# Optimization experiments

Measured on AMD Instinct MI355X. Metric: run time of the kernel, lower is better.

Reference implementation:

```python
import jax, jax.numpy as jnp
import numpy as np

B, S, F = 8, 1024, 512
E, H = 64, 16  # embed_dim per head, n_heads (match init_kwargs)


def setup_inputs() -> dict:
    key = jax.random.key(0)
    k1, k2, k3, k4, k5, k6 = jax.random.split(key, 6)
    inputs1 = jax.random.normal(k1, (B, S, F), dtype=jnp.float32)
    inputs2 = jax.random.normal(k2, (B, S, F), dtype=jnp.float32)
    W_kv = jax.random.normal(k3, (F, E * H * 2), dtype=jnp.float32) * 0.02
    b_kv = jax.random.normal(k4, (E * H * 2,), dtype=jnp.float32) * 0.02
    W_q = jax.random.normal(k5, (F, E * H), dtype=jnp.float32) * 0.02
    b_q = jax.random.normal(k6, (E * H,), dtype=jnp.float32) * 0.02
    return {"inputs1": inputs1, "inputs2": inputs2,
            "W_kv": W_kv, "b_kv": b_kv, "W_q": W_q, "b_q": b_q}


def reference(inputs1, inputs2, W_kv, b_kv, W_q, b_q):
    scaling = 1.0 / jnp.sqrt(jnp.float32(E))
    # KV path: Dense then reshape (B,S,E,H,2) -> transpose to (B,2,H,S,E)
    kv = inputs1 @ W_kv + b_kv                      # (B,S,E*H*2), layout d-major
    kv = kv.reshape(B, S, E, H, 2)
    kv = jnp.transpose(kv, (0, 4, 3, 1, 2))        # (B,2,H,S,E)
    k = kv[:, 0]                                   # (B,H,S,E)
    v = kv[:, 1]                                   # (B,H,S,E)
    # Q path: Dense then reshape (B,S,E,H) -> (B,H,S,E)
    q = (inputs2 @ W_q + b_q).reshape(B, S, E, H)
    q = jnp.transpose(q, (0, 3, 1, 2))             # (B,H,S,E)
    # Attention: softmax FIRST, then scale (non-standard, faithful to source)
    qk = jnp.einsum('bhqe,bhke->bhqk', q, k)       # (B,H,S,S)
    attn = jax.nn.softmax(qk, axis=-1) * scaling
    out = jnp.einsum('bhqk,bhke->bhqe', attn, v)   # (B,H,S,E)
    out = jnp.transpose(out, (0, 2, 1, 3))         # (B,S,H,E)
    return out.reshape(B, S, E * H)
```

## Files before the change

### kernel.cpp

```cpp
#include <hip/hip_runtime.h>
#include <hip/hip_bf16.h>
#include <math.h>

#define NB 8
#define NS 1024
#define NF 512
#define NE 64
#define NH 16

typedef __attribute__((ext_vector_type(8))) short short8;
typedef __attribute__((ext_vector_type(4))) float floatx4;

__device__ inline unsigned short f2bf(float f) {
  union { float f; unsigned int u; } c; c.f = f;
  unsigned int u = c.u;
  u += 0x7FFFu + ((u >> 16) & 1u);
  return (unsigned short)(u >> 16);
}

__device__ inline unsigned int cvt_pk_bf16(float a, float b) {
  unsigned int r;
  asm("v_cvt_pk_bf16_f32 %0, %1, %2" : "=v"(r) : "v"(a), "v"(b));
  return r;
}

__device__ inline float fexp2(float x) {
#if __has_builtin(__builtin_amdgcn_exp2f)
  return __builtin_amdgcn_exp2f(x);
#else
  return exp2f(x);
#endif
}

__device__ inline void gl_lds16(const void* g, void* l) {
  __builtin_amdgcn_global_load_lds(
      (const __attribute__((address_space(1))) unsigned int*)g,
      (__attribute__((address_space(3))) unsigned int*)l, 16, 0, 0);
}

__global__ __launch_bounds__(256) void conv_bf16(
    const float* __restrict__ in, unsigned short* __restrict__ out, int n4)
{
  int i = blockIdx.x * 256 + threadIdx.x;
  if (i < n4) {
    float4 v = ((const float4*)in)[i];
    ushort4 o;
    o.x = f2bf(v.x); o.y = f2bf(v.y); o.z = f2bf(v.z); o.w = f2bf(v.w);
    ((ushort4*)out)[i] = o;
  }
}

template <int LOGG>
__global__ __launch_bounds__(256) void perm_w(
    const float* __restrict__ W, unsigned short* __restrict__ Wt, int N)
{
  __shared__ float T[64][65];
  const int t = threadIdx.x;
  const int k0 = blockIdx.y * 64, n0 = blockIdx.x * 64;
  #pragma unroll
  for (int p = 0; p < 4; ++p) {
    int i = (t >> 4) + p * 16, j = (t & 15) * 4;
    float4 v = *(const float4*)(W + (size_t)(k0 + i) * N + n0 + j);
    T[i][j] = v.x; T[i][j + 1] = v.y; T[i][j + 2] = v.z; T[i][j + 3] = v.w;
  }
  __syncthreads();
  #pragma unroll
  for (int p = 0; p < 2; ++p) {
    int c = p * 256 + t;
    int jn = c >> 3, kc = (c & 7) * 8;
    int n = n0 + jn;
    int g = n & ((1 << LOGG) - 1), e = n >> LOGG;
    unsigned short v[8];
    #pragma unroll
    for (int j = 0; j < 8; ++j) v[j] = f2bf(T[kc + j][jn]);
    *(uint4*)(Wt + (size_t)(g * 64 + e) * NF + k0 + kc) = *(uint4*)v;
  }
}

template <int MODE>
__global__ __launch_bounds__(256) void gemm_proj(
    const unsigned short* __restrict__ A, const unsigned short* __restrict__ Wt,
    const float* __restrict__ bias, unsigned short* __restrict__ out0,
    unsigned short* __restrict__ out1)
{
  __shared__ union {
    struct { unsigned short A[2][128 * 32]; unsigned short B[2][128 * 32]; } ab;
    unsigned short C[128 * 136];
    struct { unsigned short K[128][72]; unsigned short V[64][136]; } kv;
  } u;

  const int t = threadIdx.x;
  const int w = t >> 6, l = t & 63;
  const int quad = l >> 4, l16 = l & 15;
  const int n0 = blockIdx.x * 128, m0 = blockIdx.y * 128;
  const int wm = (w >> 1) * 64, wn = (w & 1) * 64;

  floatx4 acc[4][4];
  #pragma unroll
  for (int mi = 0; mi < 4; ++mi)
    #pragma unroll
    for (int nj = 0; nj < 4; ++nj) acc[mi][nj] = (floatx4){0.f, 0.f, 0.f, 0.f};

  const unsigned short* Ag = A + (size_t)(m0 + w * 16 + (l >> 2)) * NF + (l & 3) * 8;
  const unsigned short* Bg = Wt + (size_t)(n0 + w * 16 + (l >> 2)) * NF + (l & 3) * 8;

  gl_lds16(Ag,           &u.ab.A[0][(w * 16) * 32]);
  gl_lds16(Ag + 64 * NF, &u.ab.A[0][(64 + w * 16) * 32]);
  gl_lds16(Bg,           &u.ab.B[0][(w * 16) * 32]);
  gl_lds16(Bg + 64 * NF, &u.ab.B[0][(64 + w * 16) * 32]);

  for (int kt = 0; kt < 16; ++kt) {
    __syncthreads();
    const int cur = kt & 1;
    if (kt < 15) {
      const int k0 = (kt + 1) * 32;
      gl_lds16(Ag + k0,           &u.ab.A[cur ^ 1][(w * 16) * 32]);
      gl_lds16(Ag + 64 * NF + k0, &u.ab.A[cur ^ 1][(64 + w * 16) * 32]);
      gl_lds16(Bg + k0,           &u.ab.B[cur ^ 1][(w * 16) * 32]);
      gl_lds16(Bg + 64 * NF + k0, &u.ab.B[cur ^ 1][(64 + w * 16) * 32]);
    }
    short8 af[4], bf[4];
    #pragma unroll
    for (int mi = 0; mi < 4; ++mi)
      af[mi] = *(const short8*)&u.ab.A[cur][(wm + mi * 16 + l16) * 32 + quad * 8];
    #pragma unroll
    for (int nj = 0; nj < 4; ++nj)
      bf[nj] = *(const short8*)&u.ab.B[cur][(wn + nj * 16 + l16) * 32 + quad * 8];
    #pragma unroll
    for (int mi = 0; mi < 4; ++mi)
      #pragma unroll
      for (int nj = 0; nj < 4; ++nj)
        acc[mi][nj] = __builtin_amdgcn_mfma_f32_16x16x32_bf16(
            af[mi], bf[nj], acc[mi][nj], 0, 0, 0);
  }

  float bv[4];
  #pragma unroll
  for (int nj = 0; nj < 4; ++nj) {
    int np = n0 + wn + nj * 16 + l16;
    int n = (MODE == 0) ? ((np & 63) * 32 + (np >> 6)) : ((np & 63) * 16 + (np >> 6));
    bv[nj] = bias[n];
  }
  __syncthreads();

  if (MODE == 0) {
    if (wn == 0) {
      #pragma unroll
      for (int mi = 0; mi < 4; ++mi)
        #pragma unroll
        for (int nj = 0; nj < 4; ++nj)
          #pragma unroll
          for (int r = 0; r < 4; ++r)
            u.kv.K[wm + mi * 16 + quad * 4 + r][nj * 16 + l16] =
                f2bf(acc[mi][nj][r] + bv[nj]);
    } else {
      #pragma unroll
      for (int mi = 0; mi < 4; ++mi)
        #pragma unroll
        for (int nj = 0; nj < 4; ++nj)
          #pragma unroll
          for (int r = 0; r < 4; ++r)
            u.kv.V[nj * 16 + l16][wm + mi * 16 + quad * 4 + r] =
                f2bf(acc[mi][nj][r] + bv[nj]);
    }
  } else {
    const float LOG2E = 1.44269504088896f;
    #pragma unroll
    for (int mi = 0; mi < 4; ++mi)
      #pragma unroll
      for (int nj = 0; nj < 4; ++nj)
        #pragma unroll
        for (int r = 0; r < 4; ++r)
          u.C[(wm + mi * 16 + quad * 4 + r) * 136 + wn + nj * 16 + l16] =
              f2bf((acc[mi][nj][r] + bv[nj]) * LOG2E);
  }
  __syncthreads();

  if (MODE == 0) {
    const int h = n0 >> 7, btile = m0 >> 10, s0 = m0 & 1023;
    #pragma unroll
    for (int p = 0; p < 4; ++p) {
      int c = p * 256 + t;
      int m = c >> 3, ec = c & 7;
      uint4 v = *(const uint4*)&u.kv.K[m][ec * 8];
      *(uint4*)(out0 + (((size_t)btile * NH + h) * NS + s0 + m) * NE + ec * 8) = v;
    }
    #pragma unroll
    for (int p = 0; p < 4; ++p) {
      int c = p * 256 + t;
      int e = c >> 4, mc = c & 15;
      uint4 v = *(const uint4*)&u.kv.V[e][mc * 8];
      *(uint4*)(out1 + (((size_t)btile * NH + h) * NE + e) * NS + s0 + mc * 8) = v;
    }
  } else {
    #pragma unroll
    for (int p = 0; p < 8; ++p) {
      int c = p * 256 + t;
      int m = c >> 4, col8 = (c & 15) * 8;
      uint4 v = *(const uint4*)&u.C[m * 136 + col8];
      int mg = m0 + m, b = mg >> 10, s = mg & 1023;
      int h = (n0 >> 6) + (col8 >> 6), e0 = col8 & 63;
      *(uint4*)(out0 + (((size_t)b * NH + h) * NS + s) * NE + e0) = v;
    }
  }
}

__global__ __launch_bounds__(256) void attn_kernel(
    const unsigned short* __restrict__ Q, const unsigned short* __restrict__ K,
    const unsigned short* __restrict__ Vt, float* __restrict__ out)
{
  __shared__ unsigned short Ks[2][64][64];
  __shared__ unsigned short Vs[2][64][64];

  const int t = threadIdx.x;
  const int w = t >> 6, lane = t & 63;
  const int quad = lane >> 4, l16 = lane & 15;
  const int n = blockIdx.x;
  const int qt = n >> 7;
  const int g = n & 127;
  const int h = g & 15, b = g >> 4;
  const size_t bh = ((size_t)b * NH + h) * NS * NE;

  short8 aq[2][2];
  #pragma unroll
  for (int rb = 0; rb < 2; ++rb) {
    const unsigned short* qrow =
        Q + bh + (size_t)(qt * 128 + w * 32 + rb * 16 + l16) * NE;
    aq[rb][0] = *(const short8*)(qrow + quad * 8);
    aq[rb][1] = *(const short8*)(qrow + 32 + quad * 8);
  }

  const int sr = t >> 3, sc8 = t & 7;
  const int xs = (sc8 ^ (sr & 7)) * 8;
  const int xq = (quad ^ (l16 & 7)) * 8;
  const unsigned short* Kg = K + bh;
  const unsigned short* Vg = Vt + bh;

  {
    *(uint4*)&Ks[0][sr][xs]      = *(const uint4*)(Kg + (size_t)sr * NE + sc8 * 8);
    *(uint4*)&Ks[0][32 + sr][xs] = *(const uint4*)(Kg + (size_t)(32 + sr) * NE + sc8 * 8);
    *(uint4*)&Vs[0][sr][xs]      = *(const uint4*)(Vg + (size_t)sr * NS + sc8 * 8);
    *(uint4*)&Vs[0][32 + sr][xs] = *(const uint4*)(Vg + (size_t)(32 + sr) * NS + sc8 * 8);
  }

  float lsum[2] = {0.f, 0.f};
  floatx4 O[2][4];
  #pragma unroll
  for (int rb = 0; rb < 2; ++rb)
    #pragma unroll
    for (int j = 0; j < 4; ++j) O[rb][j] = (floatx4){0.f, 0.f, 0.f, 0.f};

  for (int kt = 0; kt < NS / 64; ++kt) {
    __syncthreads();
    const int bi = kt & 1;

    uint4 kn0, kn1, vn0, vn1;
    if (kt < 15) {
      const unsigned short* kg = Kg + (size_t)(kt + 1) * 64 * NE;
      kn0 = *(const uint4*)(kg + (size_t)sr * NE + sc8 * 8);
      kn1 = *(const uint4*)(kg + (size_t)(32 + sr) * NE + sc8 * 8);
      const unsigned short* vg = Vg + (kt + 1) * 64;
      vn0 = *(const uint4*)(vg + (size_t)sr * NS + sc8 * 8);
      vn1 = *(const uint4*)(vg + (size_t)(32 + sr) * NS + sc8 * 8);
    }

    short8 kf0[4], kf1[4];
    #pragma unroll
    for (int kb = 0; kb < 4; ++kb) {
      kf0[kb] = *(const short8*)&Ks[bi][kb * 16 + l16][xq];
      kf1[kb] = *(const short8*)&Ks[bi][kb * 16 + l16][xq ^ 32];
    }

    short8 paf[2][2];
    #pragma unroll
    for (int rb = 0; rb < 2; ++rb) {
      floatx4 st[4];
      __builtin_amdgcn_s_setprio(1);
      #pragma unroll
      for (int kb = 0; kb < 4; ++kb) {
        floatx4 z = (floatx4){0.f, 0.f, 0.f, 0.f};
        z = __builtin_amdgcn_mfma_f32_16x16x32_bf16(kf0[kb], aq[rb][0], z, 0, 0, 0);
        st[kb] = __builtin_amdgcn_mfma_f32_16x16x32_bf16(kf1[kb], aq[rb][1], z, 0, 0, 0);
      }
      __builtin_amdgcn_s_setprio(0);
      unsigned int c[4][2];
      #pragma unroll
      for (int kb = 0; kb < 4; ++kb) {
        float p0 = fexp2(st[kb][0]), p1 = fexp2(st[kb][1]);
        float p2 = fexp2(st[kb][2]), p3 = fexp2(st[kb][3]);
        lsum[rb] += (p0 + p1) + (p2 + p3);
        c[kb][0] = cvt_pk_bf16(p0, p1);
        c[kb][1] = cvt_pk_bf16(p2, p3);
      }
      #pragma unroll
      for (int m = 0; m < 2; ++m) {
        union { unsigned int wd[4]; short8 v; } pu;
        #pragma unroll
        for (int j = 0; j < 2; ++j) {
          unsigned int a = c[2 * m][j], bb = c[2 * m + 1][j];
          asm("v_permlane32_swap_b32 %0, %1" : "+v"(a), "+v"(bb));
          asm("v_permlane16_swap_b32 %0, %1" : "+v"(a), "+v"(bb));
          pu.wd[j]     = a;
          pu.wd[2 + j] = bb;
        }
        paf[rb][m] = pu.v;
      }
    }

    if (kt < 15) {
      const int bn = bi ^ 1;
      *(uint4*)&Ks[bn][sr][xs]      = kn0;
      *(uint4*)&Ks[bn][32 + sr][xs] = kn1;
      *(uint4*)&Vs[bn][sr][xs]      = vn0;
      *(uint4*)&Vs[bn][32 + sr][xs] = vn1;
    }

    short8 vf0[4], vf1[4];
    #pragma unroll
    for (int eb = 0; eb < 4; ++eb) {
      vf0[eb] = *(const short8*)&Vs[bi][eb * 16 + l16][xq];
      vf1[eb] = *(const short8*)&Vs[bi][eb * 16 + l16][xq ^ 32];
    }
    __builtin_amdgcn_s_setprio(1);
    #pragma unroll
    for (int rb = 0; rb < 2; ++rb) {
      #pragma unroll
      for (int eb = 0; eb < 4; ++eb) {
        O[rb][eb] = __builtin_amdgcn_mfma_f32_16x16x32_bf16(paf[rb][0], vf0[eb], O[rb][eb], 0, 0, 0);
        O[rb][eb] = __builtin_amdgcn_mfma_f32_16x16x32_bf16(paf[rb][1], vf1[eb], O[rb][eb], 0, 0, 0);
      }
    }
    __builtin_amdgcn_s_setprio(0);
  }

  const float scaling = 0.125f;
  #pragma unroll
  for (int rb = 0; rb < 2; ++rb) {
    float lv = lsum[rb];
    lv += __shfl_xor(lv, 16);
    lv += __shfl_xor(lv, 32);
    #pragma unroll
    for (int r = 0; r < 4; ++r) {
      float inv = scaling / __shfl(lv, quad * 4 + r);
      int s = qt * 128 + w * 32 + rb * 16 + quad * 4 + r;
      float* orow = out + ((size_t)b * NS + s) * (NE * NH) + h * NE;
      orow[l16]      = O[rb][0][r] * inv;
      orow[16 + l16] = O[rb][1][r] * inv;
      orow[32 + l16] = O[rb][2][r] * inv;
      orow[48 + l16] = O[rb][3][r] * inv;
    }
  }
}

extern "C" void kernel_launch(void* const* d_in, const int* in_sizes, int n_in,
                              void* d_out, int out_size, void* d_ws, size_t ws_size,
                              hipStream_t stream) {
  const float* inputs1 = (const float*)d_in[0];
  const float* inputs2 = (const float*)d_in[1];
  const float* W_kv    = (const float*)d_in[2];
  const float* b_kv    = (const float*)d_in[3];
  const float* W_q     = (const float*)d_in[4];
  const float* b_q     = (const float*)d_in[5];
  float* out = (float*)d_out;

  const size_t plane = (size_t)NB * NH * NS * NE;
  const size_t amat  = (size_t)NB * NS * NF;
  unsigned short* Qb   = (unsigned short*)d_ws;
  unsigned short* Kb   = Qb + plane;
  unsigned short* Vtb  = Kb + plane;
  unsigned short* A1b  = Vtb + plane;
  unsigned short* A2b  = A1b + amat;
  unsigned short* Wtkv = A2b + amat;
  unsigned short* Wtq  = Wtkv + (size_t)2048 * NF;

  dim3 blk(256);
  conv_bf16<<<dim3(amat / 4 / 256), blk, 0, stream>>>(inputs1, A1b, amat / 4);
  conv_bf16<<<dim3(amat / 4 / 256), blk, 0, stream>>>(inputs2, A2b, amat / 4);
  perm_w<5><<<dim3(2048 / 64, NF / 64), blk, 0, stream>>>(W_kv, Wtkv, 2048);
  perm_w<4><<<dim3(1024 / 64, NF / 64), blk, 0, stream>>>(W_q, Wtq, 1024);
  gemm_proj<0><<<dim3(2048 / 128, 8192 / 128), blk, 0, stream>>>(
      A1b, Wtkv, b_kv, Kb, Vtb);
  gemm_proj<1><<<dim3(1024 / 128, 8192 / 128), blk, 0, stream>>>(
      A2b, Wtq, b_q, Qb, nullptr);
  attn_kernel<<<dim3(1024), blk, 0, stream>>>(Qb, Kb, Vtb, out);
}
```

Baseline: 112.6 us.

## Load attention K/V fragments directly from global memory, dropping LDS staging

Measured after the change: 181.6 us. 61.3% more time.

```diff
diff --git a/kernel.cpp b/kernel.cpp
--- a/kernel.cpp
+++ b/kernel.cpp
@@ -205,13 +205,10 @@
   }
 }
 
-__global__ __launch_bounds__(256) void attn_kernel(
+__global__ __launch_bounds__(256, 4) void attn_kernel(
     const unsigned short* __restrict__ Q, const unsigned short* __restrict__ K,
     const unsigned short* __restrict__ Vt, float* __restrict__ out)
 {
-  __shared__ unsigned short Ks[2][64][64];
-  __shared__ unsigned short Vs[2][64][64];
-
   const int t = threadIdx.x;
   const int w = t >> 6, lane = t & 63;
   const int quad = lane >> 4, l16 = lane & 15;
@@ -230,18 +227,8 @@
     aq[rb][1] = *(const short8*)(qrow + 32 + quad * 8);
   }
 
-  const int sr = t >> 3, sc8 = t & 7;
-  const int xs = (sc8 ^ (sr & 7)) * 8;
-  const int xq = (quad ^ (l16 & 7)) * 8;
-  const unsigned short* Kg = K + bh;
-  const unsigned short* Vg = Vt + bh;
-
-  {
-    *(uint4*)&Ks[0][sr][xs]      = *(const uint4*)(Kg + (size_t)sr * NE + sc8 * 8);
-    *(uint4*)&Ks[0][32 + sr][xs] = *(const uint4*)(Kg + (size_t)(32 + sr) * NE + sc8 * 8);
-    *(uint4*)&Vs[0][sr][xs]      = *(const uint4*)(Vg + (size_t)sr * NS + sc8 * 8);
-    *(uint4*)&Vs[0][32 + sr][xs] = *(const uint4*)(Vg + (size_t)(32 + sr) * NS + sc8 * 8);
-  }
+  const unsigned short* Kq = K + bh + (size_t)l16 * NE + quad * 8;
+  const unsigned short* Vq = Vt + bh + (size_t)l16 * NS + quad * 8;
 
   float lsum[2] = {0.f, 0.f};
   floatx4 O[2][4];
@@ -251,24 +238,12 @@
     for (int j = 0; j < 4; ++j) O[rb][j] = (floatx4){0.f, 0.f, 0.f, 0.f};
 
   for (int kt = 0; kt < NS / 64; ++kt) {
-    __syncthreads();
-    const int bi = kt & 1;
-
-    uint4 kn0, kn1, vn0, vn1;
-    if (kt < 15) {
-      const unsigned short* kg = Kg + (size_t)(kt + 1) * 64 * NE;
-      kn0 = *(const uint4*)(kg + (size_t)sr * NE + sc8 * 8);
-      kn1 = *(const uint4*)(kg + (size_t)(32 + sr) * NE + sc8 * 8);
-      const unsigned short* vg = Vg + (kt + 1) * 64;
-      vn0 = *(const uint4*)(vg + (size_t)sr * NS + sc8 * 8);
-      vn1 = *(const uint4*)(vg + (size_t)(32 + sr) * NS + sc8 * 8);
-    }
-
     short8 kf0[4], kf1[4];
     #pragma unroll
     for (int kb = 0; kb < 4; ++kb) {
-      kf0[kb] = *(const short8*)&Ks[bi][kb * 16 + l16][xq];
-      kf1[kb] = *(const short8*)&Ks[bi][kb * 16 + l16][xq ^ 32];
+      const unsigned short* kp = Kq + (size_t)(kt * 64 + kb * 16) * NE;
+      kf0[kb] = *(const short8*)kp;
+      kf1[kb] = *(const short8*)(kp + 32);
     }
 
     short8 paf[2][2];
@@ -307,19 +282,12 @@
       }
     }
 
-    if (kt < 15) {
-      const int bn = bi ^ 1;
-      *(uint4*)&Ks[bn][sr][xs]      = kn0;
-      *(uint4*)&Ks[bn][32 + sr][xs] = kn1;
-      *(uint4*)&Vs[bn][sr][xs]      = vn0;
-      *(uint4*)&Vs[bn][32 + sr][xs] = vn1;
-    }
-
     short8 vf0[4], vf1[4];
     #pragma unroll
     for (int eb = 0; eb < 4; ++eb) {
-      vf0[eb] = *(const short8*)&Vs[bi][eb * 16 + l16][xq];
-      vf1[eb] = *(const short8*)&Vs[bi][eb * 16 + l16][xq ^ 32];
+      const unsigned short* vp = Vq + (size_t)(eb * 16) * NS + kt * 64;
+      vf0[eb] = *(const short8*)vp;
+      vf1[eb] = *(const short8*)(vp + 32);
     }
     __builtin_amdgcn_s_setprio(1);
     #pragma unroll
```
